# Performance work log

Hardware: AMD Instinct MI355X
Metric: run time of the kernel (lower is better)

The kernel has to match this reference:

```python
import jax, jax.numpy as jnp
import numpy as np

R, M1, N1, M2, N2 = 4, 1024, 2048, 2, 4
BATCH, SEQ = 4, 2048


def setup_inputs() -> dict:
    key = jax.random.key(0)
    k_x, k_A, k_B, k_b, k_p, k_q = jax.random.split(key, 6)
    x = jax.random.normal(k_x, (BATCH, SEQ, M1 * M2), dtype=jnp.float32)
    A = jax.random.normal(k_A, (R, N1, M1), dtype=jnp.float32) * 0.001
    B = jax.random.normal(k_B, (R, M2, N2), dtype=jnp.float32) * 0.001
    b = jnp.zeros((N1 * N2,), dtype=jnp.float32)
    p_inv = jax.random.permutation(k_p, M1 * M2).astype(jnp.int32)
    q = jax.random.permutation(k_q, N1 * N2).astype(jnp.int32)
    return {"x": x, "A": A, "B": B, "b": b, "p_inv": p_inv, "q": q}


def reference(x, A, B, b, p_inv, q):
    # x: [Bt, S, m1*m2]; A: [r, n1, m1]; B: [r, m2, n2]
    r, n1, m1 = A.shape
    _, m2, n2 = B.shape
    shape = x.shape
    tokens = shape[0] * shape[1]
    # input permutation gather (use_p=True)
    xp = x[:, :, p_inv]
    # Bx = einsum('km,rmn->rkn'): [r, tokens*m1, n2]
    xf = xp.reshape(-1, m2)
    Bx = jnp.einsum('km,rmn->rkn', xf, B)
    Bx = Bx.reshape(r, tokens, m1, n2)
    # ABx = einsum('rnm,rbmj->bnj'): [tokens, n1, n2]
    ABx = jnp.einsum('rnm,rbmj->bnj', A, Bx)
    ABx = ABx.reshape(shape[:-1] + (n1 * n2,))
    # output permutation gather (use_q=True) + bias
    out = ABx[:, :, q] + b
    return out
```

## Files before the change

### kernel.cpp

```cpp
#include <hip/hip_runtime.h>
#include <hip/hip_bf16.h>

typedef unsigned short u16;
typedef __attribute__((ext_vector_type(8))) short short8;
typedef __attribute__((ext_vector_type(4))) float floatx4;

#define TOKENS 8192
#define KDIM   2048
#define NFEAT  8192
#define R_     4
#define N1_    2048
#define M1_    1024

#define BM 256
#define BN 256
#define BK 64
#define NITER (KDIM / (2 * BK))

__device__ __forceinline__ u16 f2bf(float f) {
  union { float f; unsigned u; } v; v.f = f;
  unsigned r = v.u + 0x7fffu + ((v.u >> 16) & 1u);
  return (u16)(r >> 16);
}

__global__ void k_invert_perm(const int* __restrict__ p_inv, int* __restrict__ pf) {
  int i = blockIdx.x * 256 + threadIdx.x;
  if (i < KDIM) pf[p_inv[i]] = i;
}

struct u16x4 { u16 a, b, c, d; };
__global__ void k_cvt_x(const float4* __restrict__ x4, u16x4* __restrict__ xb) {
  int i = blockIdx.x * 256 + threadIdx.x;
  float4 v = x4[i];
  u16x4 o; o.a = f2bf(v.x); o.b = f2bf(v.y); o.c = f2bf(v.z); o.d = f2bf(v.w);
  xb[i] = o;
}

__global__ void k_build_w(const float* __restrict__ A, const float* __restrict__ Bm,
                          const int* __restrict__ pf, const int* __restrict__ q,
                          u16* __restrict__ Wf) {
  int f = blockIdx.x;
  int k0 = threadIdx.x * 8;
  int qf = q[f];
  int n = qf >> 2, j = qf & 3;
  const float* An = A + (size_t)n * M1_;
  float bc[8];
#pragma unroll
  for (int r = 0; r < R_; ++r) {
    bc[r * 2 + 0] = Bm[r * 8 + 0 * 4 + j];
    bc[r * 2 + 1] = Bm[r * 8 + 1 * 4 + j];
  }
  int4 c0 = *(const int4*)(pf + k0);
  int4 c1 = *(const int4*)(pf + k0 + 4);
  int cs[8] = {c0.x, c0.y, c0.z, c0.w, c1.x, c1.y, c1.z, c1.w};
  u16 w[8];
#pragma unroll
  for (int i = 0; i < 8; ++i) {
    int m1 = cs[i] >> 1, m2 = cs[i] & 1;
    float acc = 0.f;
#pragma unroll
    for (int r = 0; r < R_; ++r)
      acc += An[(size_t)r * (N1_ * M1_) + m1] * bc[r * 2 + m2];
    w[i] = f2bf(acc);
  }
  *(short8*)(Wf + (size_t)f * KDIM + k0) = *(const short8*)w;
}

#define GLD16(gp, lp) __builtin_amdgcn_global_load_lds( \
    (const __attribute__((address_space(1))) void*)(gp), \
    (__attribute__((address_space(3))) void*)(lp), 16, 0, 0)

#define FENCE asm volatile("" ::: "memory")
#define BAR   do { FENCE; __builtin_amdgcn_s_barrier(); FENCE; } while (0)
#define LGKM0 asm volatile("s_waitcnt lgkmcnt(0)" ::: "memory")
#define VMCNT(n) asm volatile("s_waitcnt vmcnt(" #n ")" ::: "memory")

__global__ __launch_bounds__(512, 2) void k_gemm(
    const u16* __restrict__ X, const u16* __restrict__ W,
    const float* __restrict__ bias, float* __restrict__ out) {
  __shared__ __align__(16) char lds[2 * 65536];

  int bid = blockIdx.x;
  int wg  = (bid & 7) * (gridDim.x >> 3) + (bid >> 3);
  int tM = wg >> 5, tN = wg & 31;
  int rowBase = tM * BM, colBase = tN * BN;

  int tid = threadIdx.x, lane = tid & 63, wave = tid >> 6;
  int wm = wave >> 2;
  int wn = wave & 3;

  int srow = tid >> 3;
  int scol = ((tid & 7) ^ (srow & 7)) * 8;
  const u16* Asrc = X + (size_t)(rowBase + srow) * KDIM + scol;
  const u16* Bsrc = W + (size_t)(colBase + srow) * KDIM + scol;

  auto SA = [&](int slot, int half, int kt) {
#pragma unroll
    for (int jj = 0; jj < 2; ++jj)
      GLD16(Asrc + (size_t)(half * 128 + jj * 64) * KDIM + kt * 64,
            &lds[slot * 65536 + half * 16384 + jj * 8192 + tid * 16]);
  };
  auto SB = [&](int slot, int half, int kt) {
#pragma unroll
    for (int jj = 0; jj < 2; ++jj)
      GLD16(Bsrc + (size_t)(half * 128 + jj * 64) * KDIM + kt * 64,
            &lds[slot * 65536 + 32768 + half * 16384 + jj * 8192 + tid * 16]);
  };

  int l15 = lane & 15, lhi = lane >> 4, l7 = lane & 7;
  int x0 = (lhi ^ l7) * 16;
  int x1 = ((4 + lhi) ^ l7) * 16;
  int abase = wm * 16384 + l15 * 128;
  int bbase = 32768 + (wn >> 1) * 16384 + ((wn & 1) * 64 + l15) * 128;

  auto RA = [&](int slot, int m, int kk) -> short8 {
    return *(const short8*)&lds[slot * 65536 + abase + m * 2048 + (kk ? x1 : x0)];
  };
  auto RB = [&](int slot, int n, int kk) -> short8 {
    return *(const short8*)&lds[slot * 65536 + bbase + n * 2048 + (kk ? x1 : x0)];
  };

  floatx4 acc[8][4] = {};
  short8 a[4][2], a2[4][2], b[2][2], b2[2][2];

  auto RDa = [&](int slot) {
#pragma unroll
    for (int m = 0; m < 4; ++m) { a[m][0] = RA(slot, m, 0); a[m][1] = RA(slot, m, 1); }
  };
  auto RDa2 = [&](int slot) {
#pragma unroll
    for (int m = 0; m < 4; ++m) { a2[m][0] = RA(slot, 4 + m, 0); a2[m][1] = RA(slot, 4 + m, 1); }
  };
  auto RDb = [&](int slot) {
#pragma unroll
    for (int n = 0; n < 2; ++n) { b[n][0] = RB(slot, n, 0); b[n][1] = RB(slot, n, 1); }
  };
  auto RDb2 = [&](int slot) {
#pragma unroll
    for (int n = 0; n < 2; ++n) { b2[n][0] = RB(slot, 2 + n, 0); b2[n][1] = RB(slot, 2 + n, 1); }
  };

  auto MM = [&](short8 (&Af)[4][2], short8 (&Bf)[2][2], int mo, int no) {
    __builtin_amdgcn_s_setprio(1);
#pragma unroll
    for (int m = 0; m < 4; ++m)
#pragma unroll
      for (int n = 0; n < 2; ++n) {
        acc[mo + m][no + n] = __builtin_amdgcn_mfma_f32_16x16x32_bf16(Af[m][0], Bf[n][0], acc[mo + m][no + n], 0, 0, 0);
        acc[mo + m][no + n] = __builtin_amdgcn_mfma_f32_16x16x32_bf16(Af[m][1], Bf[n][1], acc[mo + m][no + n], 0, 0, 0);
      }
    __builtin_amdgcn_s_setprio(0);
  };

  SA(0, 0, 0); SA(0, 1, 0); SB(0, 0, 0); SB(0, 1, 0);
  SA(1, 0, 1); SA(1, 1, 1);
  VMCNT(4);
  BAR;
  RDa(0); RDb(0);

  for (int it = 0; it < NITER - 1; ++it) {
    int t0 = 2 * it;
    LGKM0;
    RDa2(0); SB(1, 0, t0 + 1);
    MM(a, b, 0, 0);
    BAR;
    LGKM0;
    RDb2(0); SB(1, 1, t0 + 1);
    MM(a2, b, 4, 0);
    BAR;
    LGKM0;
    SA(0, 0, t0 + 2);
    MM(a2, b2, 4, 2);
    VMCNT(2);
    BAR;
    LGKM0;
    SA(0, 1, t0 + 2);
    MM(a, b2, 0, 2);
    RDa(1); RDb(1);
    BAR;
    LGKM0;
    RDa2(1); SB(0, 0, t0 + 2);
    MM(a, b, 0, 0);
    BAR;
    LGKM0;
    RDb2(1); SB(0, 1, t0 + 2);
    MM(a2, b, 4, 0);
    BAR;
    LGKM0;
    SA(1, 0, t0 + 3);
    MM(a2, b2, 4, 2);
    VMCNT(2);
    BAR;
    LGKM0;
    SA(1, 1, t0 + 3);
    MM(a, b2, 0, 2);
    RDa(0); RDb(0);
    BAR;
  }

  {
    int t0 = 2 * (NITER - 1);
    LGKM0; RDa2(0); SB(1, 0, t0 + 1); MM(a, b, 0, 0); BAR;
    LGKM0; RDb2(0); SB(1, 1, t0 + 1); MM(a2, b, 4, 0); BAR;
    LGKM0; MM(a2, b2, 4, 2); VMCNT(0); BAR;
    LGKM0; MM(a, b2, 0, 2); RDa(1); RDb(1);
    LGKM0; RDa2(1); MM(a, b, 0, 0);
    LGKM0; RDb2(1); MM(a2, b, 4, 0);
    LGKM0; MM(a2, b2, 4, 2);
    MM(a, b2, 0, 2);
  }

  float bv[4];
#pragma unroll
  for (int n = 0; n < 4; ++n)
    bv[n] = bias[colBase + wn * 64 + n * 16 + l15];
#pragma unroll
  for (int m = 0; m < 8; ++m) {
    int r0 = wm * 128 + m * 16 + (lhi << 2);
#pragma unroll
    for (int n = 0; n < 4; ++n) {
      size_t basep = (size_t)(rowBase + r0) * NFEAT + colBase + wn * 64 + n * 16 + l15;
#pragma unroll
      for (int reg = 0; reg < 4; ++reg)
        out[basep + (size_t)reg * NFEAT] = acc[m][n][reg] + bv[n];
    }
  }
}

extern "C" void kernel_launch(void* const* d_in, const int* in_sizes, int n_in,
                              void* d_out, int out_size, void* d_ws, size_t ws_size,
                              hipStream_t stream) {
  const float* x     = (const float*)d_in[0];
  const float* A     = (const float*)d_in[1];
  const float* Bm    = (const float*)d_in[2];
  const float* bias  = (const float*)d_in[3];
  const int*   p_inv = (const int*)d_in[4];
  const int*   q     = (const int*)d_in[5];
  float* out = (float*)d_out;

  u16* Xb = (u16*)d_ws;
  u16* Wf = (u16*)((char*)d_ws + (size_t)TOKENS * KDIM * 2);
  int* pf = (int*)((char*)d_ws + (size_t)TOKENS * KDIM * 2 * 2);

  k_invert_perm<<<(KDIM + 255) / 256, 256, 0, stream>>>(p_inv, pf);
  k_cvt_x<<<(TOKENS * KDIM / 4) / 256, 256, 0, stream>>>((const float4*)x, (u16x4*)Xb);
  k_build_w<<<NFEAT, 256, 0, stream>>>(A, Bm, pf, q, Wf);
  k_gemm<<<(TOKENS / BM) * (NFEAT / BN), 512, 0, stream>>>(Xb, Wf, bias, out);
}
```

Measured before the change: 333.2 us.

## Restructure GEMM main loop into uniform phases with in-loop tail handling

Changes the ping-pong GEMM main loop so each phase issues LDS reads and global-to-LDS prefetches, then waits at a barrier before the MFMA block. The last iteration is folded into the loop under a `full` flag, replacing the separate epilogue. The goal is a more regular schedule and safer ordering, but it adds extra barriers per phase and removes the overlap of LDS reads with the previous MFMA block, which can lengthen the critical path.

```diff
diff --git a/kernel.cpp b/kernel.cpp
--- a/kernel.cpp
+++ b/kernel.cpp
@@ -156,58 +156,49 @@
   SA(1, 0, 1); SA(1, 1, 1);
   VMCNT(4);
   BAR;
-  RDa(0); RDb(0);
-
-  for (int it = 0; it < NITER - 1; ++it) {
+
+  for (int it = 0; it < NITER; ++it) {
     int t0 = 2 * it;
-    LGKM0;
-    RDa2(0); SB(1, 0, t0 + 1);
+    bool full = (it < NITER - 1);
+
+    RDa(0); RDb(0);
+    SB(1, 0, t0 + 1);
+    BAR; LGKM0;
     MM(a, b, 0, 0);
     BAR;
-    LGKM0;
-    RDb2(0); SB(1, 1, t0 + 1);
+    RDa2(0);
+    SB(1, 1, t0 + 1);
+    BAR; LGKM0;
     MM(a2, b, 4, 0);
     BAR;
-    LGKM0;
-    SA(0, 0, t0 + 2);
+    RDb2(0);
+    if (full) SA(0, 0, t0 + 2);
+    BAR; LGKM0;
     MM(a2, b2, 4, 2);
-    VMCNT(2);
-    BAR;
-    LGKM0;
-    SA(0, 1, t0 + 2);
+    BAR;
+    if (full) { SA(0, 1, t0 + 2); VMCNT(4); } else { VMCNT(0); }
+    BAR;
     MM(a, b2, 0, 2);
+    BAR;
     RDa(1); RDb(1);
-    BAR;
-    LGKM0;
-    RDa2(1); SB(0, 0, t0 + 2);
+    if (full) SB(0, 0, t0 + 2);
+    BAR; LGKM0;
     MM(a, b, 0, 0);
     BAR;
-    LGKM0;
-    RDb2(1); SB(0, 1, t0 + 2);
+    RDa2(1);
+    if (full) SB(0, 1, t0 + 2);
+    BAR; LGKM0;
     MM(a2, b, 4, 0);
     BAR;
-    LGKM0;
-    SA(1, 0, t0 + 3);
+    RDb2(1);
+    if (full) SA(1, 0, t0 + 3);
+    BAR; LGKM0;
     MM(a2, b2, 4, 2);
-    VMCNT(2);
-    BAR;
-    LGKM0;
-    SA(1, 1, t0 + 3);
+    BAR;
+    if (full) { SA(1, 1, t0 + 3); VMCNT(4); }
+    BAR;
     MM(a, b2, 0, 2);
-    RDa(0); RDb(0);
-    BAR;
-  }
-
-  {
-    int t0 = 2 * (NITER - 1);
-    LGKM0; RDa2(0); SB(1, 0, t0 + 1); MM(a, b, 0, 0); BAR;
-    LGKM0; RDb2(0); SB(1, 1, t0 + 1); MM(a2, b, 4, 0); BAR;
-    LGKM0; MM(a2, b2, 4, 2); VMCNT(0); BAR;
-    LGKM0; MM(a, b2, 0, 2); RDa(1); RDb(1);
-    LGKM0; RDa2(1); MM(a, b, 0, 0);
-    LGKM0; RDb2(1); MM(a2, b, 4, 0);
-    LGKM0; MM(a2, b2, 4, 2);
-    MM(a, b2, 0, 2);
+    BAR;
   }
 
   float bv[4];
```

New measurement: 346.0 us. 1.04x slower.
